# Performance work log

Hardware: AMD Instinct MI355X
Metric: run time of the kernel (lower is better)

## Reference

```python
import jax, jax.numpy as jnp
import numpy as np
import math

# Model dims (match init_kwargs)
N = 2048      # columns
DS = 64       # d_state
DI = 256      # d_input
DV = 64       # d_vote
K = 512       # k_active = int(N * 0.25)
H = 4         # bus attention heads
HD = DV // H  # head dim
MULT = 4
B, T = 2, 4


def _rmsnorm(x, w, eps=1e-6):
    return w * x * jax.lax.rsqrt(jnp.mean(x * x, axis=-1, keepdims=True) + eps)


def setup_inputs() -> dict:
    key = jax.random.key(0)
    ks = jax.random.split(key, 12)
    s = 0.02
    dcat = DS + DS + DV  # concat[h, x, m]
    return {
        "x": jax.random.normal(ks[0], (B, T, DI), jnp.float32),
        "W_in": jax.random.normal(ks[1], (DS, DI), jnp.float32) * s,
        "core_norm_w": jnp.ones((dcat,), jnp.float32),
        "core_Wg": jax.random.normal(ks[2], (2 * MULT * DS, dcat), jnp.float32) * s,
        "core_Wout": jax.random.normal(ks[3], (DS, MULT * DS), jnp.float32) * s,
        "W_gate": jax.random.normal(ks[4], (1, DS), jnp.float32) * s,
        "W_vote": jax.random.normal(ks[5], (DV, DS), jnp.float32) * s,
        "attn_in_w": jax.random.normal(ks[6], (3 * DV, DV), jnp.float32) * s,
        "attn_out_w": jax.random.normal(ks[7], (DV, DV), jnp.float32) * s,
        "W_film_scale": jax.random.normal(ks[8], (DS, DV), jnp.float32) * s,
        "W_film_shift": jax.random.normal(ks[9], (DS, DV), jnp.float32) * s,
        "query": jax.random.normal(ks[10], (1, 1, DS), jnp.float32),
        "out_norm_w": jnp.ones((DS,), jnp.float32),
        "W_out": jax.random.normal(ks[11], (DI, DS), jnp.float32) * s,
    }


def _forward(x, W_in, core_norm_w, core_Wg, core_Wout, W_gate, W_vote,
             attn_in_w, attn_out_w, W_film_scale, W_film_shift, query,
             out_norm_w, W_out):
    Bsz = x.shape[0]
    Wq, Wk, Wv = jnp.split(attn_in_w, 3, axis=0)
    bidx = jnp.arange(Bsz)[:, None]

    def step(h, x_t):
        # input projection, broadcast to every column
        x_proj = x_t @ W_in.T                                     # (B, DS)
        x_rep = jnp.broadcast_to(x_proj[:, None, :], (Bsz, N, DS))
        # top-k gating with straight-through soft scores
        gate = jnp.squeeze(h @ W_gate.T, -1)                      # (B, N)
        _, idx = jax.lax.top_k(gate, K)
        mask_hard = jnp.zeros((Bsz, N), x.dtype).at[bidx, idx].set(1.0)
        mask_soft = jax.nn.softmax(gate, axis=-1)
        ms = (mask_hard + mask_soft - jax.lax.stop_gradient(mask_soft))[..., None]
        # column core: RMSNorm -> SwiGLU -> proj -> residual (m = zeros)
        z = _rmsnorm(jnp.concatenate(
            [h, x_rep, jnp.zeros((Bsz, N, DV), x.dtype)], axis=-1), core_norm_w)
        a, b = jnp.split(z @ core_Wg.T, 2, axis=-1)
        h_hat = h + (a * jax.nn.silu(b)) @ core_Wout.T
        h = h + ms * (h_hat - h)
        # votes, masked to active columns
        v = (h @ W_vote.T) * ms                                   # (B, N, DV)
        # bus self-attention with key padding mask on inactive columns
        qh = (v @ Wq.T).reshape(Bsz, N, H, HD)
        kh = (v @ Wk.T).reshape(Bsz, N, H, HD)
        vh = (v @ Wv.T).reshape(Bsz, N, H, HD)
        logits = jnp.einsum('bqhd,bkhd->bhqk', qh, kh) / math.sqrt(HD)
        pad = mask_hard == 0.0
        logits = jnp.where(pad[:, None, None, :], -jnp.inf, logits)
        attnw = jax.nn.softmax(logits, axis=-1)
        m = jnp.einsum('bhqk,bkhd->bqhd', attnw, vh).reshape(Bsz, N, DV) @ attn_out_w.T
        # FiLM modulation
        h = h * (1.0 + jnp.tanh(m @ W_film_scale.T)) + m @ W_film_shift.T
        # learned-query pooling over columns
        pl = jnp.einsum('d,bnd->bn', query[0, 0], h) / math.sqrt(DS)
        pw = jax.nn.softmax(pl, axis=-1)
        pooled = jnp.einsum('bn,bnd->bd', pw, h)
        y = _rmsnorm(pooled, out_norm_w) @ W_out.T               # (B, DI)
        return h, y

    h0 = jnp.zeros((Bsz, N, DS), x.dtype)  # fresh state per forward (reset_state)
    _, ys = jax.lax.scan(step, h0, jnp.swapaxes(x, 0, 1))
    return jnp.swapaxes(ys, 0, 1)  # (B, T, DI)


def reference(x, W_in, core_norm_w, core_Wg, core_Wout, W_gate, W_vote,
              attn_in_w, attn_out_w, W_film_scale, W_film_shift, query,
              out_norm_w, W_out):
    return _forward(x, W_in, core_norm_w, core_Wg, core_Wout, W_gate, W_vote,
                    attn_in_w, attn_out_w, W_film_scale, W_film_shift, query,
                    out_norm_w, W_out)
```

## Files before the change

### kernel.cpp

```cpp
#include <hip/hip_runtime.h>
#include <hip/hip_bf16.h>

#define NN 2048
#define DS 64
#define DI 256
#define DV 64
#define KK 512
#define HH 4
#define HD 16
#define BB 2
#define TT 4
#define DCAT 192

typedef unsigned long long ull;

__device__ __forceinline__ float wave_sum(float v) {
#pragma unroll
    for (int o = 32; o > 0; o >>= 1) v += __shfl_xor(v, o);
    return v;
}
__device__ __forceinline__ float wave_max(float v) {
#pragma unroll
    for (int o = 32; o > 0; o >>= 1) v = fmaxf(v, __shfl_xor(v, o));
    return v;
}
__device__ __forceinline__ unsigned enc_f(float f) {
    unsigned u = __float_as_uint(f);
    return (u & 0x80000000u) ? ~u : (u | 0x80000000u);
}

__global__ __launch_bounds__(256) void k_head(
    const float* __restrict__ gate, const float* __restrict__ x,
    const float* __restrict__ W_in, int* __restrict__ col2slot,
    int* __restrict__ act_idx, float* __restrict__ xproj,
    const float* __restrict__ ppool, const float* __restrict__ psum,
    const float* __restrict__ pmax, const float* __restrict__ onw,
    const float* __restrict__ W_out, float* __restrict__ out, int t)
{
    __shared__ char smem[20992];
    int blk = blockIdx.x, tid = threadIdx.x;
    if (blk < 2) {
        if (t >= TT) return;
        int b = blk;
        {
            int r = tid >> 2, q = tid & 3;
            const float* xp = x + (b * TT + t) * DI + q * 64;
            const float* wr = W_in + r * DI + q * 64;
            float a = 0.f;
#pragma unroll
            for (int i = 0; i < 64; i++) a += xp[i] * wr[i];
            a += __shfl_xor(a, 1); a += __shfl_xor(a, 2);
            if (q == 0) xproj[b * DS + r] = a;
        }
        if (t == 0) {
            for (int i = tid; i < NN; i += 256) col2slot[b * NN + i] = (i < KK) ? i : -1;
            for (int i = tid; i < KK; i += 256) act_idx[b * KK + i] = i;
            return;
        }
        ull* keys = (ull*)smem;
        unsigned* hist = (unsigned*)(smem + 16384);
        unsigned* suf  = (unsigned*)(smem + 17408);
        ull* pref_sh   = (ull*)(smem + 18432);
        int* need_sh   = (int*)(smem + 18440);
        unsigned* ccnt = (unsigned*)(smem + 18444);
        if (tid == 0) *ccnt = 0;
        for (int i = tid; i < NN; i += 256) {
            keys[i] = ((ull)enc_f(gate[b * NN + i]) << 11) | (unsigned)(NN - 1 - i);
            col2slot[b * NN + i] = -1;
        }
        ull prefix = 0, pmask = 0;
        int need = KK;
        for (int shift = 40; shift >= 0; shift -= 8) {
            hist[tid] = 0;
            __syncthreads();
            for (int i = tid; i < NN; i += 256) {
                ull k = keys[i];
                if ((k & pmask) == prefix)
                    atomicAdd(&hist[(unsigned)((k >> shift) & 255)], 1u);
            }
            __syncthreads();
            suf[tid] = hist[tid];
            __syncthreads();
            for (int s = 1; s < 256; s <<= 1) {
                unsigned v = (tid + s < 256) ? suf[tid + s] : 0u;
                __syncthreads();
                suf[tid] += v;
                __syncthreads();
            }
            {
                unsigned here = suf[tid];
                unsigned above = (tid == 255) ? 0u : suf[tid + 1];
                if (here >= (unsigned)need && above < (unsigned)need) {
                    *pref_sh = prefix | ((ull)tid << shift);
                    *need_sh = need - (int)above;
                }
            }
            __syncthreads();
            prefix = *pref_sh; need = *need_sh; pmask |= (0xFFull << shift);
            __syncthreads();
        }
        for (int i = tid; i < NN; i += 256) {
            ull k = keys[i];
            if (k >= prefix) {
                unsigned p = atomicAdd(ccnt, 1u);
                int n = NN - 1 - (int)(k & 2047ull);
                act_idx[b * KK + p] = n;
                col2slot[b * NN + n] = (int)p;
            }
        }
    } else {
        if (t == 0) return;
        int b = blk - 2;
        float* pn = (float*)(smem + 20480);
        if (tid < 64) {
            int d = tid;
            float gm = -1e30f;
            for (int i = 0; i < 64; i++) gm = fmaxf(gm, pmax[b * 64 + i]);
            float s = 0.f, v = 0.f;
            for (int i = 0; i < 64; i++) {
                float e = __expf(pmax[b * 64 + i] - gm);
                s += psum[b * 64 + i] * e;
                v += ppool[(b * 64 + i) * 64 + d] * e;
            }
            float val = v / s;
            float ss = wave_sum(val * val);
            float rs = rsqrtf(ss * (1.0f / DS) + 1e-6f);
            pn[d] = onw[d] * val * rs;
        }
        __syncthreads();
        {
            int o = tid;
            const float* wr = W_out + o * DS;
            float a = 0.f;
#pragma unroll
            for (int d = 0; d < DS; d++) a += pn[d] * wr[d];
            out[(b * TT + (t - 1)) * DI + o] = a;
        }
    }
}

__global__ __launch_bounds__(256) void k_core_a(
    const float* __restrict__ h, const float* __restrict__ xproj,
    const int* __restrict__ act_idx, const float* __restrict__ norm_w,
    const float* __restrict__ Wg, float* __restrict__ u_g)
{
    __shared__ float zt[128 * 64];
    __shared__ float ssq[4 * 64];
    __shared__ float rsb[64];
    int cg = blockIdx.x >> 4;
    int og = blockIdx.x & 15;
    int tid = threadIdx.x;
    int c = tid & 63;
    int seg = __builtin_amdgcn_readfirstlane(tid >> 6);
    int b = cg >> 3;
    int sbase = (cg & 7) * 64;
    int n = act_idx[b * KK + sbase + c];
    float vals[32];
    float sq = 0.f;
    if (seg < 2) {
        const float* hp = h + ((size_t)(b * NN + n)) * DS + seg * 32;
#pragma unroll
        for (int i = 0; i < 32; i++) { float v = hp[i]; vals[i] = v; sq += v * v; }
    } else {
        const float* xp = xproj + b * DS + (seg - 2) * 32;
#pragma unroll
        for (int i = 0; i < 32; i++) { float v = xp[i]; vals[i] = v; sq += v * v; }
    }
    ssq[seg * 64 + c] = sq;
    __syncthreads();
    if (tid < 64) {
        float s = ssq[tid] + ssq[64 + tid] + ssq[128 + tid] + ssq[192 + tid];
        rsb[tid] = rsqrtf(s * (1.0f / DCAT) + 1e-6f);
    }
    __syncthreads();
    {
        float rs = rsb[c];
#pragma unroll
        for (int i = 0; i < 32; i++) {
            int d = seg * 32 + i;
            zt[d * 64 + c] = norm_w[d] * vals[i] * rs;
        }
    }
    __syncthreads();
    float z[128];
#pragma unroll
    for (int d = 0; d < 128; d++) z[d] = zt[d * 64 + c];
    int rbase = og * 16 + seg * 4;
    float ga[4];
#pragma unroll
    for (int r = 0; r < 4; r++) {
        const float* wr = Wg + (rbase + r) * DCAT;
        float acc = 0.f;
#pragma unroll
        for (int d = 0; d < 128; d++) acc += z[d] * wr[d];
        ga[r] = acc;
    }
    int gcol = cg * 64 + c;
#pragma unroll
    for (int r = 0; r < 4; r++) {
        const float* wr = Wg + (256 + rbase + r) * DCAT;
        float bacc = 0.f;
#pragma unroll
        for (int d = 0; d < 128; d++) bacc += z[d] * wr[d];
        float uu = ga[r] * (bacc / (1.f + expf(-bacc)));
        u_g[(rbase + r) * 1024 + gcol] = uu;
    }
}

__global__ __launch_bounds__(256) void k_hupd(
    const float* __restrict__ u_g, const float* __restrict__ Wout,
    float* __restrict__ part)
{
    __shared__ float tile[64 * 65];
    int blk = blockIdx.x;
    int cg = blk >> 2, kc = blk & 3;
    int tid = threadIdx.x;
    int c = tid & 63, w = tid >> 6;
    int gcolbase = cg * 64;
    float uu[64];
#pragma unroll
    for (int i = 0; i < 64; i++) uu[i] = u_g[(kc * 64 + i) * 1024 + gcolbase + c];
#pragma unroll
    for (int oi = 0; oi < 16; oi++) {
        int o = w * 16 + oi;
        const float* wr = Wout + o * 256 + kc * 64;
        float acc = 0.f;
#pragma unroll
        for (int i = 0; i < 64; i++) acc += uu[i] * wr[i];
        tile[o * 65 + c] = acc;
    }
    __syncthreads();
#pragma unroll
    for (int k = 0; k < 16; k++) {
        int flat = k * 256 + tid;
        int gl = flat >> 6, oo = flat & 63;
        part[(size_t)(gcolbase + gl) * 256 + kc * 64 + oo] = tile[oo * 65 + gl];
    }
}

__global__ __launch_bounds__(256) void k_vqkv(
    float* __restrict__ h, const float* __restrict__ part,
    const int* __restrict__ act_idx,
    const float* __restrict__ W_vote, const float* __restrict__ attn_in_w,
    float* __restrict__ qh, float* __restrict__ kh, float* __restrict__ vh)
{
    __shared__ float hn[64 * 33];
    __shared__ float vv[64 * 33];
    __shared__ int an[32];
    int blk = blockIdx.x;
    int b = blk >> 4;
    int sbase = (blk & 15) * 32;
    int tid = threadIdx.x;
    int w = __builtin_amdgcn_readfirstlane(tid >> 6);
    int l = tid & 63;
    int c = l & 31, sub = l >> 5;
    if (tid < 32) an[tid] = act_idx[b * KK + sbase + tid];
    __syncthreads();
    {
        int o = tid & 63;
#pragma unroll
        for (int k = 0; k < 8; k++) {
            int s = (tid >> 6) + k * 4;
            const float* pp = part + (size_t)(b * KK + sbase + s) * 256 + o;
            float sum = pp[0] + pp[64] + pp[128] + pp[192];
            size_t hidx = ((size_t)(b * NN + an[s])) * DS + o;
            float nh = h[hidx] + sum;
            h[hidx] = nh;
            hn[o * 33 + s] = nh;
        }
    }
    __syncthreads();
    float hh[32];
#pragma unroll
    for (int i = 0; i < 32; i++) hh[i] = hn[(sub * 32 + i) * 33 + c];
#pragma unroll 4
    for (int oi = 0; oi < 16; oi++) {
        int o = w * 16 + oi;
        const float* wr = W_vote + o * 64 + sub * 32;
        float a = 0.f;
#pragma unroll
        for (int i = 0; i < 32; i++) a += hh[i] * wr[i];
        a += __shfl_xor(a, 32);
        if (sub == 0) vv[o * 33 + c] = a;
    }
    __syncthreads();
    float vq[32];
#pragma unroll
    for (int i = 0; i < 32; i++) vq[i] = vv[(sub * 32 + i) * 33 + c];
    int slot = sbase + c;
#pragma unroll 4
    for (int oi = 0; oi < 48; oi++) {
        int r = w * 48 + oi;
        const float* wr = attn_in_w + r * 64 + sub * 32;
        float a = 0.f;
#pragma unroll
        for (int i = 0; i < 32; i++) a += vq[i] * wr[i];
        a += __shfl_xor(a, 32);
        if (sub == 0) {
            if (r < 64) {
                qh[((b * HH + (r >> 4)) * KK + slot) * HD + (r & 15)] = a;
            } else if (r < 128) {
                int rr = r - 64;
                kh[((b * HH + (rr >> 4)) * HD + (rr & 15)) * KK + slot] = a;
            } else {
                int rr = r - 128;
                vh[((b * HH + (rr >> 4)) * HD + (rr & 15)) * KK + slot] = a;
            }
        }
    }
}

__global__ __launch_bounds__(256) void k_attn(
    const float* __restrict__ qh, const float* __restrict__ kh,
    const float* __restrict__ vh, float* __restrict__ m_raw)
{
    int wave = threadIdx.x >> 6, lane = threadIdx.x & 63;
    int task = blockIdx.x * 4 + wave;
    int qs = task & (KK - 1);
    int bh = task >> 9;
    const float* qp = qh + (bh * KK + qs) * HD;
    float q[HD];
#pragma unroll
    for (int d = 0; d < HD; d++) q[d] = qp[d];
    const float* kp = kh + bh * HD * KK;
    const float* vp = vh + bh * HD * KK;
    float lg[8]; float mx = -1e30f;
#pragma unroll
    for (int i = 0; i < 8; i++) {
        int slot = i * 64 + lane;
        float a = 0.f;
#pragma unroll
        for (int d = 0; d < HD; d++) a += q[d] * kp[d * KK + slot];
        lg[i] = a * 0.25f;
        mx = fmaxf(mx, lg[i]);
    }
    mx = wave_max(mx);
    float p[8]; float sum = 0.f;
#pragma unroll
    for (int i = 0; i < 8; i++) { p[i] = __expf(lg[i] - mx); sum += p[i]; }
    sum = wave_sum(sum);
    float inv = 1.0f / sum;
    float acc[HD];
#pragma unroll
    for (int d = 0; d < HD; d++) acc[d] = 0.f;
#pragma unroll
    for (int i = 0; i < 8; i++) {
        int slot = i * 64 + lane;
        float pi = p[i];
#pragma unroll
        for (int d = 0; d < HD; d++) acc[d] += pi * vp[d * KK + slot];
    }
#pragma unroll
    for (int d = 0; d < HD; d++) acc[d] = wave_sum(acc[d]) * inv;
    if (lane == 0) {
        int b = bh >> 2, head = bh & 3;
#pragma unroll
        for (int d = 0; d < HD; d++)
            m_raw[(b * DV + head * HD + d) * KK + qs] = acc[d];
    }
}

__global__ __launch_bounds__(256) void k_film2(
    float* __restrict__ h, const int* __restrict__ act_idx,
    const float* __restrict__ m_raw, const float* __restrict__ vh,
    const float* __restrict__ attn_out_w, const float* __restrict__ Wfs,
    const float* __restrict__ Wfsh, float* __restrict__ fsm, float* __restrict__ fshm)
{
    __shared__ char smem[33152];
    int blk = blockIdx.x;
    int tid = threadIdx.x;
    if (blk < 32) {
        float* mt  = (float*)smem;
        float* mot = (float*)(smem + 8192);
        float* sct = (float*)(smem + 16384);
        float* sht = (float*)(smem + 24704);
        int* an    = (int*)(smem + 33024);
        int b = blk >> 4;
        int sbase = (blk & 15) * 32;
        int w = __builtin_amdgcn_readfirstlane(tid >> 6);
        int lane = tid & 63;
        int s = lane & 31, half = lane >> 5;
        if (tid < 32) an[tid] = act_idx[b * KK + sbase + tid];
        for (int idx = tid; idx < 2048; idx += 256) {
            int d = idx >> 5, ss = idx & 31;
            mt[d * 32 + ss] = m_raw[(b * DV + d) * KK + sbase + ss];
        }
        __syncthreads();
#pragma unroll 4
        for (int oi = 0; oi < 16; oi++) {
            int o = w * 16 + oi;
            const float* wr = attn_out_w + o * DV + half * 32;
            float a = 0.f;
#pragma unroll
            for (int e = 0; e < 32; e++) a += mt[(half * 32 + e) * 32 + s] * wr[e];
            a += __shfl_xor(a, 32);
            if (half == 0) mot[o * 32 + s] = a;
        }
        __syncthreads();
#pragma unroll 4
        for (int oi = 0; oi < 16; oi++) {
            int o = w * 16 + oi;
            const float* ws_ = Wfs + o * DV + half * 32;
            const float* wh_ = Wfsh + o * DV + half * 32;
            float sc = 0.f, sh = 0.f;
#pragma unroll
            for (int e = 0; e < 32; e++) {
                float zz = mot[(half * 32 + e) * 32 + s];
                sc += ws_[e] * zz; sh += wh_[e] * zz;
            }
            sc += __shfl_xor(sc, 32); sh += __shfl_xor(sh, 32);
            if (half == 0) { sct[s * 65 + o] = tanhf(sc); sht[s * 65 + o] = sh; }
        }
        __syncthreads();
        for (int idx = tid; idx < 2048; idx += 256) {
            int o = idx & 63, ss = idx >> 6;
            size_t hix = ((size_t)(b * NN + an[ss])) * DS + o;
            h[hix] = h[hix] * (1.f + sct[ss * 65 + o]) + sht[ss * 65 + o];
        }
    } else {
        int b = blk - 32;
        float* partm = (float*)smem;
        float* mr = (float*)(smem + 1024);
        float* mo2 = (float*)(smem + 1280);
        int w = tid >> 6, lane = tid & 63;
        float macc[64];
#pragma unroll
        for (int d = 0; d < 64; d++) macc[d] = 0.f;
        for (int s = tid; s < KK; s += 256) {
#pragma unroll
            for (int d = 0; d < 64; d++) macc[d] += vh[(b * DV + d) * KK + s];
        }
#pragma unroll
        for (int d = 0; d < 64; d++) macc[d] = wave_sum(macc[d]);
        if (lane == 0) {
#pragma unroll
            for (int d = 0; d < 64; d++) partm[w * 64 + d] = macc[d];
        }
        __syncthreads();
        if (tid < 64)
            mr[tid] = (partm[tid] + partm[64 + tid] + partm[128 + tid] + partm[192 + tid]) * (1.0f / KK);
        __syncthreads();
        if (tid < 64) {
            const float* wo = attn_out_w + tid * DV;
            float a = 0.f;
#pragma unroll
            for (int e = 0; e < 64; e++) a += mr[e] * wo[e];
            mo2[tid] = a;
        }
        __syncthreads();
        if (tid < 64) {
            const float* ws_ = Wfs + tid * DV;
            const float* wh_ = Wfsh + tid * DV;
            float sc = 0.f, sh = 0.f;
#pragma unroll
            for (int e = 0; e < 64; e++) { float zz = mo2[e]; sc += ws_[e] * zz; sh += wh_[e] * zz; }
            fsm[b * DS + tid] = tanhf(sc);
            fshm[b * DS + tid] = sh;
        }
    }
}

__global__ __launch_bounds__(256) void k_pool2(
    float* __restrict__ h, const int* __restrict__ col2slot,
    const float* __restrict__ fsm, const float* __restrict__ fshm,
    const float* __restrict__ query, const float* __restrict__ W_gate,
    float* __restrict__ gate, float* __restrict__ ppool,
    float* __restrict__ psum, float* __restrict__ pmax)
{
    __shared__ float wvecs[4][64];
    __shared__ float wms[4], wss[4];
    int blk = blockIdx.x;
    int b = blk >> 6;
    int base = (blk & 63) * 32;
    int tid = threadIdx.x;
    int w = tid >> 6, lane = tid & 63;
    float fs = fsm[b * DS + lane], fh = fshm[b * DS + lane];
    float qv = query[lane] * 0.125f, wg = W_gate[lane];
    float wm = -1e30f, sw = 0.f, vec = 0.f;
#pragma unroll
    for (int ci = 0; ci < 8; ci++) {
        int n = base + w * 8 + ci;
        size_t idx = ((size_t)(b * NN + n)) * DS + lane;
        float hv = h[idx];
        int slot = col2slot[b * NN + n];
        if (slot < 0) { hv = hv * (1.f + fs) + fh; h[idx] = hv; }
        float lg = wave_sum(qv * hv);
        float gt = wave_sum(wg * hv);
        if (lane == 0) gate[b * NN + n] = gt;
        float nm = fmaxf(wm, lg);
        float scale = __expf(wm - nm);
        float e = __expf(lg - nm);
        sw = sw * scale + e;
        vec = vec * scale + e * hv;
        wm = nm;
    }
    wvecs[w][lane] = vec;
    if (lane == 0) { wms[w] = wm; wss[w] = sw; }
    __syncthreads();
    if (tid < 64) {
        float m4 = fmaxf(fmaxf(wms[0], wms[1]), fmaxf(wms[2], wms[3]));
        float s = 0.f, v = 0.f;
#pragma unroll
        for (int ww = 0; ww < 4; ww++) {
            float e = __expf(wms[ww] - m4);
            s += wss[ww] * e;
            v += wvecs[ww][tid] * e;
        }
        ppool[blk * 64 + tid] = v;
        if (tid == 0) { psum[blk] = s; pmax[blk] = m4; }
    }
}

extern "C" void kernel_launch(void* const* d_in, const int* in_sizes, int n_in,
                              void* d_out, int out_size, void* d_ws, size_t ws_size,
                              hipStream_t stream)
{
    const float* x          = (const float*)d_in[0];
    const float* W_in       = (const float*)d_in[1];
    const float* core_norm_w= (const float*)d_in[2];
    const float* core_Wg    = (const float*)d_in[3];
    const float* core_Wout  = (const float*)d_in[4];
    const float* W_gate     = (const float*)d_in[5];
    const float* W_vote     = (const float*)d_in[6];
    const float* attn_in_w  = (const float*)d_in[7];
    const float* attn_out_w = (const float*)d_in[8];
    const float* Wfs        = (const float*)d_in[9];
    const float* Wfsh       = (const float*)d_in[10];
    const float* query      = (const float*)d_in[11];
    const float* onw        = (const float*)d_in[12];
    const float* W_out      = (const float*)d_in[13];
    float* out = (float*)d_out;

    float* ws = (float*)d_ws;
    float* h        = ws;
    float* gate     = h + (size_t)BB * NN * DS;
    float* xproj    = gate + BB * NN;
    int*   col2slot = (int*)(xproj + BB * DS);
    int*   act_idx  = col2slot + BB * NN;
    float* u_g      = (float*)(act_idx + BB * KK);
    float* part     = u_g + 256 * 1024;
    float* qh       = part + 256 * 1024;
    float* kh       = qh + BB * HH * KK * HD;
    float* vh       = kh + BB * HH * KK * HD;
    float* m_raw    = vh + BB * HH * KK * HD;
    float* fsm      = m_raw + BB * DV * KK;
    float* fshm     = fsm + BB * DS;
    float* ppool    = fshm + BB * DS;
    float* psum     = ppool + 128 * 64;
    float* pmax     = psum + 128;

    hipMemsetAsync(h, 0, ((size_t)BB * NN * DS + BB * NN) * sizeof(float), stream);

    for (int t = 0; t < TT; t++) {
        k_head<<<4, 256, 0, stream>>>(gate, x, W_in, col2slot, act_idx, xproj,
                                      ppool, psum, pmax, onw, W_out, out, t);
        k_core_a<<<256, 256, 0, stream>>>(h, xproj, act_idx, core_norm_w, core_Wg, u_g);
        k_hupd<<<64, 256, 0, stream>>>(u_g, core_Wout, part);
        k_vqkv<<<32, 256, 0, stream>>>(h, part, act_idx, W_vote, attn_in_w, qh, kh, vh);
        k_attn<<<BB * HH * KK / 4, 256, 0, stream>>>(qh, kh, vh, m_raw);
        k_film2<<<34, 256, 0, stream>>>(h, act_idx, m_raw, vh, attn_out_w, Wfs, Wfsh, fsm, fshm);
        k_pool2<<<128, 256, 0, stream>>>(h, col2slot, fsm, fshm, query, W_gate, gate, ppool, psum, pmax);
    }
    k_head<<<4, 256, 0, stream>>>(gate, x, W_in, col2slot, act_idx, xproj,
                                  ppool, psum, pmax, onw, W_out, out, TT);
}
```

Measured before the change: 412.7 us.

## Fuse head into pool via last-block atomic, merge hupd with vqkv, hoist xproj

Moves the per-step input projection and first-step init into a single pre-kernel, folds the k_hupd partial-sum kernel into the QKV projection kernel (k_coreb, 16 blocks of 512 threads), and moves the top-k selection and output pooling into the last finishing block of k_pool2 using an atomic counter. The aim is to cut kernel launches per step from 7 to 5, drop the 'part' intermediate buffer round trip, and remove the serialized 4-block head kernel. The trade-off is that k_coreb runs on only 16 blocks, so the Wout matmul parallelism drops, and the top-k now runs serially inside one tail block of the pool kernel. The q layout also changes to head-dim-major to match the k and v layouts.

Result: slower. 531.9 us (+28.9%).

```diff
diff --git a/kernel.cpp b/kernel.cpp
--- a/kernel.cpp
+++ b/kernel.cpp
@@ -29,120 +29,32 @@
     return (u & 0x80000000u) ? ~u : (u | 0x80000000u);
 }
 
-__global__ __launch_bounds__(256) void k_head(
-    const float* __restrict__ gate, const float* __restrict__ x,
-    const float* __restrict__ W_in, int* __restrict__ col2slot,
-    int* __restrict__ act_idx, float* __restrict__ xproj,
-    const float* __restrict__ ppool, const float* __restrict__ psum,
-    const float* __restrict__ pmax, const float* __restrict__ onw,
-    const float* __restrict__ W_out, float* __restrict__ out, int t)
-{
-    __shared__ char smem[20992];
+__global__ __launch_bounds__(256) void k_pre(
+    const float* __restrict__ x, const float* __restrict__ W_in,
+    float* __restrict__ xproj, int* __restrict__ col2slot, int* __restrict__ act_idx)
+{
     int blk = blockIdx.x, tid = threadIdx.x;
-    if (blk < 2) {
-        if (t >= TT) return;
-        int b = blk;
-        {
-            int r = tid >> 2, q = tid & 3;
-            const float* xp = x + (b * TT + t) * DI + q * 64;
-            const float* wr = W_in + r * DI + q * 64;
-            float a = 0.f;
-#pragma unroll
-            for (int i = 0; i < 64; i++) a += xp[i] * wr[i];
-            a += __shfl_xor(a, 1); a += __shfl_xor(a, 2);
-            if (q == 0) xproj[b * DS + r] = a;
-        }
-        if (t == 0) {
-            for (int i = tid; i < NN; i += 256) col2slot[b * NN + i] = (i < KK) ? i : -1;
-            for (int i = tid; i < KK; i += 256) act_idx[b * KK + i] = i;
-            return;
-        }
-        ull* keys = (ull*)smem;
-        unsigned* hist = (unsigned*)(smem + 16384);
-        unsigned* suf  = (unsigned*)(smem + 17408);
-        ull* pref_sh   = (ull*)(smem + 18432);
-        int* need_sh   = (int*)(smem + 18440);
-        unsigned* ccnt = (unsigned*)(smem + 18444);
-        if (tid == 0) *ccnt = 0;
-        for (int i = tid; i < NN; i += 256) {
-            keys[i] = ((ull)enc_f(gate[b * NN + i]) << 11) | (unsigned)(NN - 1 - i);
-            col2slot[b * NN + i] = -1;
-        }
-        ull prefix = 0, pmask = 0;
-        int need = KK;
-        for (int shift = 40; shift >= 0; shift -= 8) {
-            hist[tid] = 0;
-            __syncthreads();
-            for (int i = tid; i < NN; i += 256) {
-                ull k = keys[i];
-                if ((k & pmask) == prefix)
-                    atomicAdd(&hist[(unsigned)((k >> shift) & 255)], 1u);
-            }
-            __syncthreads();
-            suf[tid] = hist[tid];
-            __syncthreads();
-            for (int s = 1; s < 256; s <<= 1) {
-                unsigned v = (tid + s < 256) ? suf[tid + s] : 0u;
-                __syncthreads();
-                suf[tid] += v;
-                __syncthreads();
-            }
-            {
-                unsigned here = suf[tid];
-                unsigned above = (tid == 255) ? 0u : suf[tid + 1];
-                if (here >= (unsigned)need && above < (unsigned)need) {
-                    *pref_sh = prefix | ((ull)tid << shift);
-                    *need_sh = need - (int)above;
-                }
-            }
-            __syncthreads();
-            prefix = *pref_sh; need = *need_sh; pmask |= (0xFFull << shift);
-            __syncthreads();
-        }
-        for (int i = tid; i < NN; i += 256) {
-            ull k = keys[i];
-            if (k >= prefix) {
-                unsigned p = atomicAdd(ccnt, 1u);
-                int n = NN - 1 - (int)(k & 2047ull);
-                act_idx[b * KK + p] = n;
-                col2slot[b * NN + n] = (int)p;
-            }
-        }
+    if (blk < 8) {
+        int b = blk >> 2, t = blk & 3;
+        int r = tid >> 2, q = tid & 3;
+        const float* xp = x + (b * TT + t) * DI + q * 64;
+        const float* wr = W_in + r * DI + q * 64;
+        float a = 0.f;
+#pragma unroll
+        for (int i = 0; i < 64; i++) a += xp[i] * wr[i];
+        a += __shfl_xor(a, 1); a += __shfl_xor(a, 2);
+        if (q == 0) xproj[(b * TT + t) * DS + r] = a;
     } else {
-        if (t == 0) return;
-        int b = blk - 2;
-        float* pn = (float*)(smem + 20480);
-        if (tid < 64) {
-            int d = tid;
-            float gm = -1e30f;
-            for (int i = 0; i < 64; i++) gm = fmaxf(gm, pmax[b * 64 + i]);
-            float s = 0.f, v = 0.f;
-            for (int i = 0; i < 64; i++) {
-                float e = __expf(pmax[b * 64 + i] - gm);
-                s += psum[b * 64 + i] * e;
-                v += ppool[(b * 64 + i) * 64 + d] * e;
-            }
-            float val = v / s;
-            float ss = wave_sum(val * val);
-            float rs = rsqrtf(ss * (1.0f / DS) + 1e-6f);
-            pn[d] = onw[d] * val * rs;
-        }
-        __syncthreads();
-        {
-            int o = tid;
-            const float* wr = W_out + o * DS;
-            float a = 0.f;
-#pragma unroll
-            for (int d = 0; d < DS; d++) a += pn[d] * wr[d];
-            out[(b * TT + (t - 1)) * DI + o] = a;
-        }
+        int b = blk - 8;
+        for (int i = tid; i < NN; i += 256) col2slot[b * NN + i] = (i < KK) ? i : -1;
+        for (int i = tid; i < KK; i += 256) act_idx[b * KK + i] = i;
     }
 }
 
 __global__ __launch_bounds__(256) void k_core_a(
     const float* __restrict__ h, const float* __restrict__ xproj,
     const int* __restrict__ act_idx, const float* __restrict__ norm_w,
-    const float* __restrict__ Wg, float* __restrict__ u_g)
+    const float* __restrict__ Wg, float* __restrict__ u_g, int t)
 {
     __shared__ float zt[128 * 64];
     __shared__ float ssq[4 * 64];
@@ -162,7 +74,7 @@
 #pragma unroll
         for (int i = 0; i < 32; i++) { float v = hp[i]; vals[i] = v; sq += v * v; }
     } else {
-        const float* xp = xproj + b * DS + (seg - 2) * 32;
+        const float* xp = xproj + (b * TT + t) * DS + (seg - 2) * 32;
 #pragma unroll
         for (int i = 0; i < 32; i++) { float v = xp[i]; vals[i] = v; sq += v * v; }
     }
@@ -207,105 +119,85 @@
     }
 }
 
-__global__ __launch_bounds__(256) void k_hupd(
-    const float* __restrict__ u_g, const float* __restrict__ Wout,
-    float* __restrict__ part)
-{
-    __shared__ float tile[64 * 65];
-    int blk = blockIdx.x;
-    int cg = blk >> 2, kc = blk & 3;
-    int tid = threadIdx.x;
-    int c = tid & 63, w = tid >> 6;
-    int gcolbase = cg * 64;
-    float uu[64];
-#pragma unroll
-    for (int i = 0; i < 64; i++) uu[i] = u_g[(kc * 64 + i) * 1024 + gcolbase + c];
-#pragma unroll
-    for (int oi = 0; oi < 16; oi++) {
-        int o = w * 16 + oi;
-        const float* wr = Wout + o * 256 + kc * 64;
-        float acc = 0.f;
-#pragma unroll
-        for (int i = 0; i < 64; i++) acc += uu[i] * wr[i];
-        tile[o * 65 + c] = acc;
-    }
-    __syncthreads();
-#pragma unroll
-    for (int k = 0; k < 16; k++) {
-        int flat = k * 256 + tid;
-        int gl = flat >> 6, oo = flat & 63;
-        part[(size_t)(gcolbase + gl) * 256 + kc * 64 + oo] = tile[oo * 65 + gl];
-    }
-}
-
-__global__ __launch_bounds__(256) void k_vqkv(
-    float* __restrict__ h, const float* __restrict__ part,
-    const int* __restrict__ act_idx,
+__global__ __launch_bounds__(512) void k_coreb(
+    float* __restrict__ h, const float* __restrict__ u_g,
+    const int* __restrict__ act_idx, const float* __restrict__ Wout,
     const float* __restrict__ W_vote, const float* __restrict__ attn_in_w,
     float* __restrict__ qh, float* __restrict__ kh, float* __restrict__ vh)
 {
-    __shared__ float hn[64 * 33];
-    __shared__ float vv[64 * 33];
-    __shared__ int an[32];
-    int blk = blockIdx.x;
-    int b = blk >> 4;
-    int sbase = (blk & 15) * 32;
-    int tid = threadIdx.x;
+    __shared__ float u_lds[64 * 64];
+    __shared__ float hn[64 * 65];
+    __shared__ float vv[64 * 65];
+    __shared__ int an[64];
+    int blk = blockIdx.x, tid = threadIdx.x;
+    int b = blk >> 3, sbase = (blk & 7) * 64;
+    int c = tid & 63;
     int w = __builtin_amdgcn_readfirstlane(tid >> 6);
-    int l = tid & 63;
-    int c = l & 31, sub = l >> 5;
-    if (tid < 32) an[tid] = act_idx[b * KK + sbase + tid];
+    if (tid < 64) an[tid] = act_idx[b * KK + sbase + tid];
+    float acc[8];
+#pragma unroll
+    for (int i = 0; i < 8; i++) acc[i] = 0.f;
+    for (int ch = 0; ch < 4; ch++) {
+        __syncthreads();
+#pragma unroll
+        for (int k = 0; k < 8; k++) {
+            int idx = k * 512 + tid;
+            int row = idx >> 6, cc = idx & 63;
+            u_lds[row * 64 + cc] = u_g[(ch * 64 + row) * 1024 + b * KK + sbase + cc];
+        }
+        __syncthreads();
+#pragma unroll
+        for (int oi = 0; oi < 8; oi++) {
+            int o = w * 8 + oi;
+            const float* wr = Wout + o * 256 + ch * 64;
+            float a = 0.f;
+#pragma unroll
+            for (int r = 0; r < 64; r++) a += u_lds[r * 64 + c] * wr[r];
+            acc[oi] += a;
+        }
+    }
+    __syncthreads();
+#pragma unroll
+    for (int oi = 0; oi < 8; oi++) hn[(w * 8 + oi) * 65 + c] = acc[oi];
     __syncthreads();
     {
         int o = tid & 63;
 #pragma unroll
         for (int k = 0; k < 8; k++) {
-            int s = (tid >> 6) + k * 4;
-            const float* pp = part + (size_t)(b * KK + sbase + s) * 256 + o;
-            float sum = pp[0] + pp[64] + pp[128] + pp[192];
+            int s = w * 8 + k;
             size_t hidx = ((size_t)(b * NN + an[s])) * DS + o;
-            float nh = h[hidx] + sum;
+            float nh = h[hidx] + hn[o * 65 + s];
             h[hidx] = nh;
-            hn[o * 33 + s] = nh;
-        }
-    }
-    __syncthreads();
-    float hh[32];
-#pragma unroll
-    for (int i = 0; i < 32; i++) hh[i] = hn[(sub * 32 + i) * 33 + c];
-#pragma unroll 4
-    for (int oi = 0; oi < 16; oi++) {
-        int o = w * 16 + oi;
-        const float* wr = W_vote + o * 64 + sub * 32;
+            hn[o * 65 + s] = nh;
+        }
+    }
+    __syncthreads();
+#pragma unroll
+    for (int oi = 0; oi < 8; oi++) {
+        int o = w * 8 + oi;
+        const float* wr = W_vote + o * 64;
         float a = 0.f;
 #pragma unroll
-        for (int i = 0; i < 32; i++) a += hh[i] * wr[i];
-        a += __shfl_xor(a, 32);
-        if (sub == 0) vv[o * 33 + c] = a;
-    }
-    __syncthreads();
-    float vq[32];
-#pragma unroll
-    for (int i = 0; i < 32; i++) vq[i] = vv[(sub * 32 + i) * 33 + c];
+        for (int r = 0; r < 64; r++) a += hn[r * 65 + c] * wr[r];
+        vv[o * 65 + c] = a;
+    }
+    __syncthreads();
     int slot = sbase + c;
 #pragma unroll 4
-    for (int oi = 0; oi < 48; oi++) {
-        int r = w * 48 + oi;
-        const float* wr = attn_in_w + r * 64 + sub * 32;
+    for (int oi = 0; oi < 24; oi++) {
+        int r = w * 24 + oi;
+        const float* wr = attn_in_w + r * 64;
         float a = 0.f;
 #pragma unroll
-        for (int i = 0; i < 32; i++) a += vq[i] * wr[i];
-        a += __shfl_xor(a, 32);
-        if (sub == 0) {
-            if (r < 64) {
-                qh[((b * HH + (r >> 4)) * KK + slot) * HD + (r & 15)] = a;
-            } else if (r < 128) {
-                int rr = r - 64;
-                kh[((b * HH + (rr >> 4)) * HD + (rr & 15)) * KK + slot] = a;
-            } else {
-                int rr = r - 128;
-                vh[((b * HH + (rr >> 4)) * HD + (rr & 15)) * KK + slot] = a;
-            }
+        for (int e = 0; e < 64; e++) a += vv[e * 65 + c] * wr[e];
+        if (r < 64) {
+            qh[((b * HH + (r >> 4)) * HD + (r & 15)) * KK + slot] = a;
+        } else if (r < 128) {
+            int rr = r - 64;
+            kh[((b * HH + (rr >> 4)) * HD + (rr & 15)) * KK + slot] = a;
+        } else {
+            int rr = r - 128;
+            vh[((b * HH + (rr >> 4)) * HD + (rr & 15)) * KK + slot] = a;
         }
     }
 }
@@ -318,10 +210,9 @@
     int task = blockIdx.x * 4 + wave;
     int qs = task & (KK - 1);
     int bh = task >> 9;
-    const float* qp = qh + (bh * KK + qs) * HD;
     float q[HD];
 #pragma unroll
-    for (int d = 0; d < HD; d++) q[d] = qp[d];
+    for (int d = 0; d < HD; d++) q[d] = qh[(bh * HD + d) * KK + qs];
     const float* kp = kh + bh * HD * KK;
     const float* vp = vh + bh * HD * KK;
     float lg[8]; float mx = -1e30f;
@@ -461,14 +352,22 @@
 }
 
 __global__ __launch_bounds__(256) void k_pool2(
-    float* __restrict__ h, const int* __restrict__ col2slot,
+    float* __restrict__ h, int* __restrict__ col2slot,
     const float* __restrict__ fsm, const float* __restrict__ fshm,
     const float* __restrict__ query, const float* __restrict__ W_gate,
     float* __restrict__ gate, float* __restrict__ ppool,
-    float* __restrict__ psum, float* __restrict__ pmax)
+    float* __restrict__ psum, float* __restrict__ pmax,
+    unsigned* __restrict__ done, const float* __restrict__ onw,
+    const float* __restrict__ W_out, float* __restrict__ out,
+    int* __restrict__ act_idx, int t)
 {
     __shared__ float wvecs[4][64];
     __shared__ float wms[4], wss[4];
+    __shared__ int lastsh;
+    __shared__ ull keys[NN];
+    __shared__ unsigned hist[256], suf[256];
+    __shared__ ull pref_sh; __shared__ int need_sh; __shared__ unsigned ccnt;
+    __shared__ float pn[64];
     int blk = blockIdx.x;
     int b = blk >> 6;
     int base = (blk & 63) * 32;
@@ -509,6 +408,84 @@
         ppool[blk * 64 + tid] = v;
         if (tid == 0) { psum[blk] = s; pmax[blk] = m4; }
     }
+    __syncthreads();
+    if (tid == 0) {
+        unsigned old = __hip_atomic_fetch_add(&done[t * BB + b], 1u,
+                                              __ATOMIC_ACQ_REL, __HIP_MEMORY_SCOPE_AGENT);
+        lastsh = (old == 63);
+    }
+    __syncthreads();
+    if (!lastsh) return;
+    if (tid < 64) {
+        int d = tid;
+        float gm = -1e30f;
+        for (int i = 0; i < 64; i++) gm = fmaxf(gm, pmax[b * 64 + i]);
+        float s = 0.f, v = 0.f;
+        for (int i = 0; i < 64; i++) {
+            float e = __expf(pmax[b * 64 + i] - gm);
+            s += psum[b * 64 + i] * e;
+            v += ppool[(b * 64 + i) * 64 + d] * e;
+        }
+        float val = v / s;
+        float ss = wave_sum(val * val);
+        float rs = rsqrtf(ss * (1.0f / DS) + 1e-6f);
+        pn[d] = onw[d] * val * rs;
+    }
+    __syncthreads();
+    {
+        int o = tid;
+        const float* wr = W_out + o * DS;
+        float a = 0.f;
+#pragma unroll
+        for (int d = 0; d < DS; d++) a += pn[d] * wr[d];
+        out[(b * TT + t) * DI + o] = a;
+    }
+    if (t == TT - 1) return;
+    if (tid == 0) ccnt = 0;
+    for (int i = tid; i < NN; i += 256) {
+        keys[i] = ((ull)enc_f(gate[b * NN + i]) << 11) | (unsigned)(NN - 1 - i);
+        col2slot[b * NN + i] = -1;
+    }
+    ull prefix = 0, pmask = 0;
+    int need = KK;
+    for (int shift = 40; shift >= 0; shift -= 8) {
+        hist[tid] = 0;
+        __syncthreads();
+        for (int i = tid; i < NN; i += 256) {
+            ull k = keys[i];
+            if ((k & pmask) == prefix)
+                atomicAdd(&hist[(unsigned)((k >> shift) & 255)], 1u);
+        }
+        __syncthreads();
+        suf[tid] = hist[tid];
+        __syncthreads();
+        for (int s = 1; s < 256; s <<= 1) {
+            unsigned v = (tid + s < 256) ? suf[tid + s] : 0u;
+            __syncthreads();
+            suf[tid] += v;
+            __syncthreads();
+        }
+        {
+            unsigned here = suf[tid];
+            unsigned above = (tid == 255) ? 0u : suf[tid + 1];
+            if (here >= (unsigned)need && above < (unsigned)need) {
+                pref_sh = prefix | ((ull)tid << shift);
+                need_sh = need - (int)above;
+            }
+        }
+        __syncthreads();
+        prefix = pref_sh; need = need_sh; pmask |= (0xFFull << shift);
+        __syncthreads();
+    }
+    for (int i = tid; i < NN; i += 256) {
+        ull k = keys[i];
+        if (k >= prefix) {
+            unsigned p = atomicAdd(&ccnt, 1u);
+            int n = NN - 1 - (int)(k & 2047ull);
+            act_idx[b * KK + p] = n;
+            col2slot[b * NN + n] = (int)p;
+        }
+    }
 }
 
 extern "C" void kernel_launch(void* const* d_in, const int* in_sizes, int n_in,
@@ -534,12 +511,12 @@
     float* ws = (float*)d_ws;
     float* h        = ws;
     float* gate     = h + (size_t)BB * NN * DS;
-    float* xproj    = gate + BB * NN;
-    int*   col2slot = (int*)(xproj + BB * DS);
+    unsigned* done  = (unsigned*)(gate + BB * NN);
+    float* xproj    = (float*)(done + 16);
+    int*   col2slot = (int*)(xproj + BB * TT * DS);
     int*   act_idx  = col2slot + BB * NN;
     float* u_g      = (float*)(act_idx + BB * KK);
-    float* part     = u_g + 256 * 1024;
-    float* qh       = part + 256 * 1024;
+    float* qh       = u_g + 256 * 1024;
     float* kh       = qh + BB * HH * KK * HD;
     float* vh       = kh + BB * HH * KK * HD;
     float* m_raw    = vh + BB * HH * KK * HD;
@@ -549,18 +526,15 @@
     float* psum     = ppool + 128 * 64;
     float* pmax     = psum + 128;
 
-    hipMemsetAsync(h, 0, ((size_t)BB * NN * DS + BB * NN) * sizeof(float), stream);
-
+    hipMemsetAsync(h, 0, ((size_t)BB * NN * DS + BB * NN + 16) * sizeof(float), stream);
+
+    k_pre<<<10, 256, 0, stream>>>(x, W_in, xproj, col2slot, act_idx);
     for (int t = 0; t < TT; t++) {
-        k_head<<<4, 256, 0, stream>>>(gate, x, W_in, col2slot, act_idx, xproj,
-                                      ppool, psum, pmax, onw, W_out, out, t);
-        k_core_a<<<256, 256, 0, stream>>>(h, xproj, act_idx, core_norm_w, core_Wg, u_g);
-        k_hupd<<<64, 256, 0, stream>>>(u_g, core_Wout, part);
-        k_vqkv<<<32, 256, 0, stream>>>(h, part, act_idx, W_vote, attn_in_w, qh, kh, vh);
+        k_core_a<<<256, 256, 0, stream>>>(h, xproj, act_idx, core_norm_w, core_Wg, u_g, t);
+        k_coreb<<<16, 512, 0, stream>>>(h, u_g, act_idx, core_Wout, W_vote, attn_in_w, qh, kh, vh);
         k_attn<<<BB * HH * KK / 4, 256, 0, stream>>>(qh, kh, vh, m_raw);
         k_film2<<<34, 256, 0, stream>>>(h, act_idx, m_raw, vh, attn_out_w, Wfs, Wfsh, fsm, fshm);
-        k_pool2<<<128, 256, 0, stream>>>(h, col2slot, fsm, fshm, query, W_gate, gate, ppool, psum, pmax);
-    }
-    k_head<<<4, 256, 0, stream>>>(gate, x, W_in, col2slot, act_idx, xproj,
-                                  ppool, psum, pmax, onw, W_out, out, TT);
-}
+        k_pool2<<<128, 256, 0, stream>>>(h, col2slot, fsm, fshm, query, W_gate, gate,
+                                         ppool, psum, pmax, done, onw, W_out, out, act_idx, t);
+    }
+}
```
